# Optimization experiments

Hardware: AMD Instinct MI355X
Metric: run time of the kernel (lower is better)

Reference implementation:

```python
import jax, jax.numpy as jnp
import numpy as np

B, S, D = 2, 2048, 4096
H, G, HD = 32, 8, 128          # num_heads, num_kv_groups, head_dim
GROUP = H // G                  # group_size = 4
SCALE = HD ** -0.5


def setup_inputs() -> dict:
    key = jax.random.key(0)
    ks = jax.random.split(key, 6)
    x = jax.random.normal(ks[0], (B, S, D), dtype=jnp.float32)
    # Linear weights stored as [in, out] (y = x @ W), no bias, 0.02 init scale
    Wq = jax.random.normal(ks[1], (D, H * HD), dtype=jnp.float32) * 0.02
    Wk = jax.random.normal(ks[2], (D, G * HD), dtype=jnp.float32) * 0.02
    Wv = jax.random.normal(ks[3], (D, G * HD), dtype=jnp.float32) * 0.02
    Wo = jax.random.normal(ks[4], (H * HD, D), dtype=jnp.float32) * 0.02
    # RoPE tables: [S, HD], duplicated-half layout (rotate-half convention)
    inv_freq = 1.0 / (10000.0 ** (jnp.arange(0, HD, 2, dtype=jnp.float32) / HD))
    angles = jnp.arange(S, dtype=jnp.float32)[:, None] * inv_freq[None, :]  # [S, HD/2]
    angles = jnp.concatenate([angles, angles], axis=-1)                      # [S, HD]
    cos = jnp.cos(angles)
    sin = jnp.sin(angles)
    # causal mask: True = masked (strict upper triangle)
    mask = jnp.triu(jnp.ones((S, S), dtype=bool), k=1)
    return {"x": x, "Wq": Wq, "Wk": Wk, "Wv": Wv, "Wo": Wo,
            "cos": cos, "sin": sin, "mask": mask, "start_pos": 0}


def _rope(t, cos, sin, offset):
    # t: [B, h, S, HD]; cos/sin: [S_total, HD]
    n = t.shape[2]
    c = jax.lax.dynamic_slice_in_dim(cos, offset, n, axis=0)  # [n, HD]
    s = jax.lax.dynamic_slice_in_dim(sin, offset, n, axis=0)
    t1, t2 = t[..., : HD // 2], t[..., HD // 2:]
    rotated = jnp.concatenate([-t2, t1], axis=-1)
    return t * c[None, None] + rotated * s[None, None]


def reference(x, Wq, Wk, Wv, Wo, cos, sin, mask, start_pos):
    # projections
    q = (x @ Wq).reshape(B, S, H, HD).transpose(0, 2, 1, 3)   # [B,H,S,HD]
    k = (x @ Wk).reshape(B, S, G, HD).transpose(0, 2, 1, 3)   # [B,G,S,HD]
    v = (x @ Wv).reshape(B, S, G, HD).transpose(0, 2, 1, 3)   # [B,G,S,HD]
    # RoPE (no cache: prev_len = 0)
    q = _rope(q, cos, sin, start_pos) * SCALE
    k = _rope(k, cos, sin, start_pos)
    # GQA: expand kv groups to full heads (repeat_interleave along head dim)
    k_r = jnp.repeat(k, GROUP, axis=1)                         # [B,H,S,HD]
    v_r = jnp.repeat(v, GROUP, axis=1)
    scores = jnp.einsum('bhqd,bhkd->bhqk', q, k_r)             # [B,H,S,S]
    scores = jnp.where(mask[None, None], -jnp.inf, scores)
    w = jax.nn.softmax(scores, axis=-1)
    ctx = jnp.einsum('bhqk,bhkd->bhqd', w, v_r)                # [B,H,S,HD]
    ctx = ctx.transpose(0, 2, 1, 3).reshape(B, S, H * HD)
    out = ctx @ Wo                                             # [B,S,D]
    return out
```

## Files before the change

kernel.cpp:

```cpp
#include <hip/hip_runtime.h>
#include <hip/hip_bf16.h>
#include <math.h>

#define B_ 2
#define S_ 2048
#define D_ 4096
#define H_ 32
#define G_ 8
#define HD_ 128
#define GROUP_ 4
#define KVSTR_ (2 * G_ * HD_)
#define SCALE_ 0.08838834764831845f

typedef short bfv8 __attribute__((ext_vector_type(8)));
typedef float f32x4 __attribute__((ext_vector_type(4)));

__device__ __forceinline__ f32x4 mfma16(bfv8 a, bfv8 b, f32x4 c) {
  return __builtin_amdgcn_mfma_f32_16x16x32_bf16(a, b, c, 0, 0, 0);
}

__device__ __forceinline__ ushort f2bf_bits(float f) {
  __hip_bfloat16 h = __float2bfloat16(f);
  return *reinterpret_cast<ushort*>(&h);
}

__device__ __forceinline__ void gload16(const short* g, short* l) {
  __builtin_amdgcn_global_load_lds(
      (const __attribute__((address_space(1))) void*)g,
      (__attribute__((address_space(3))) void*)l, 16, 0, 0);
}

__global__ __launch_bounds__(256) void k_cvt(const float* __restrict__ in,
                                             ushort* __restrict__ out, int n4) {
  int i = blockIdx.x * 256 + threadIdx.x;
  if (i >= n4) return;
  float4 v = *(const float4*)(in + (size_t)i * 4);
  ushort4 o;
  o.x = f2bf_bits(v.x); o.y = f2bf_bits(v.y); o.z = f2bf_bits(v.z); o.w = f2bf_bits(v.w);
  *(ushort4*)(out + (size_t)i * 4) = o;
}

__global__ __launch_bounds__(256) void k_transpose(const float* __restrict__ in,
                                                   ushort* __restrict__ out,
                                                   int R, int C) {
  __shared__ ushort tile[32][36];
  int bc = blockIdx.x * 32;
  int br = blockIdx.y * 32;
  int t = threadIdx.x;
  int rr = t >> 3;
  int c4 = (t & 7) * 4;
  float4 v = *(const float4*)(in + (size_t)(br + rr) * C + bc + c4);
  tile[rr][c4 + 0] = f2bf_bits(v.x);
  tile[rr][c4 + 1] = f2bf_bits(v.y);
  tile[rr][c4 + 2] = f2bf_bits(v.z);
  tile[rr][c4 + 3] = f2bf_bits(v.w);
  __syncthreads();
  int cc = t >> 3;
  int r4 = (t & 7) * 4;
  ushort4 o;
  o.x = tile[r4 + 0][cc];
  o.y = tile[r4 + 1][cc];
  o.z = tile[r4 + 2][cc];
  o.w = tile[r4 + 3][cc];
  *(ushort4*)(out + (size_t)(bc + cc) * R + br + r4) = o;
}

__global__ __launch_bounds__(256) void k_transpose_v(const ushort* __restrict__ v,
                                                     ushort* __restrict__ vt,
                                                     int hstride, int hoff) {
  __shared__ ushort tile[32][33];
  int bg = blockIdx.z;
  int b = bg / G_, g = bg % G_;
  int s0 = blockIdx.y * 32;
  int h0 = blockIdx.x * 32;
  int tx = threadIdx.x, ty = threadIdx.y;
  const ushort* src = v + (size_t)b * S_ * hstride + (size_t)(hoff + g) * HD_;
  ushort* dst = vt + (size_t)(b * G_ + g) * HD_ * S_;
  for (int ii = 0; ii < 4; ii++) {
    int i = ty + ii * 8;
    tile[i][tx] = src[(size_t)(s0 + i) * hstride + h0 + tx];
  }
  __syncthreads();
  for (int ii = 0; ii < 4; ii++) {
    int i = ty + ii * 8;
    dst[(size_t)(h0 + i) * S_ + s0 + tx] = tile[tx][i];
  }
}

__global__ __launch_bounds__(256) void k_rope(__hip_bfloat16* __restrict__ t,
                                              const float* __restrict__ cosb,
                                              const float* __restrict__ sinb,
                                              int hstride, int nlaunch, float scale) {
  int item = blockIdx.x * 4 + (threadIdx.x >> 6);
  int head = item % nlaunch;
  int row = item / nlaunch;
  int s = row & (S_ - 1);
  int l = threadIdx.x & 63;
  size_t base = (size_t)row * hstride * HD_ + (size_t)head * HD_;
  float x1 = __bfloat162float(t[base + l]);
  float x2 = __bfloat162float(t[base + 64 + l]);
  float c1 = cosb[s * HD_ + l];
  float sn1 = sinb[s * HD_ + l];
  float c2 = cosb[s * HD_ + 64 + l];
  float sn2 = sinb[s * HD_ + 64 + l];
  t[base + l] = __float2bfloat16((x1 * c1 - x2 * sn1) * scale);
  t[base + 64 + l] = __float2bfloat16((x2 * c2 + x1 * sn2) * scale);
}

template <typename OT>
__global__ __launch_bounds__(256) void k_gemm_bt(const __hip_bfloat16* __restrict__ Ab,
                                                 const __hip_bfloat16* __restrict__ BTb,
                                                 OT* __restrict__ Cb,
                                                 int M, int N, int K) {
  __shared__ short sA[128 * 32];
  __shared__ short sB[128 * 32];
  int t = threadIdx.x;
  int w = t >> 6;
  int l = t & 63;
  int row0 = blockIdx.y * 128;
  int col0 = blockIdx.x * 128;
  int wr = (w >> 1) * 64;
  int wc = (w & 1) * 64;
  int fr = l & 15;
  int fq = l >> 4;
  int fo = fq * 8;
  int srow = l >> 2;
  int schk = (l & 3) * 8;

  const short* gA = (const short*)Ab;
  const short* gB = (const short*)BTb;

  f32x4 acc[4][4];
#pragma unroll
  for (int m = 0; m < 4; m++)
#pragma unroll
    for (int n = 0; n < 4; n++) acc[m][n] = (f32x4){0.f, 0.f, 0.f, 0.f};

  for (int k0 = 0; k0 < K; k0 += 32) {
    __syncthreads();
#pragma unroll
    for (int j = 0; j < 2; j++) {
      int r = w * 32 + j * 16;
      gload16(gA + (size_t)(row0 + r + srow) * K + k0 + schk, &sA[r * 32]);
      gload16(gB + (size_t)(col0 + r + srow) * K + k0 + schk, &sB[r * 32]);
    }
    __syncthreads();
    bfv8 af[4], bff[4];
#pragma unroll
    for (int m = 0; m < 4; m++) af[m] = *(const bfv8*)(sA + (wr + m * 16 + fr) * 32 + fo);
#pragma unroll
    for (int n = 0; n < 4; n++) bff[n] = *(const bfv8*)(sB + (wc + n * 16 + fr) * 32 + fo);
#pragma unroll
    for (int m = 0; m < 4; m++)
#pragma unroll
      for (int n = 0; n < 4; n++)
        acc[m][n] = mfma16(af[m], bff[n], acc[m][n]);
  }
#pragma unroll
  for (int m = 0; m < 4; m++)
#pragma unroll
    for (int n = 0; n < 4; n++)
#pragma unroll
      for (int j = 0; j < 4; j++) {
        int r = row0 + wr + m * 16 + fq * 4 + j;
        int c = col0 + wc + n * 16 + fr;
        if constexpr (__is_same(OT, float)) {
          Cb[(size_t)r * N + c] = acc[m][n][j];
        } else {
          Cb[(size_t)r * N + c] = __float2bfloat16(acc[m][n][j]);
        }
      }
}

template <typename OT>
__global__ __launch_bounds__(512, 2) void k_gemm256(const __hip_bfloat16* __restrict__ Ab,
                                                    const __hip_bfloat16* __restrict__ BTb,
                                                    OT* __restrict__ Cb,
                                                    int M, int N, int K) {
  __shared__ short sA[2][2][8192];
  __shared__ short sB[2][2][8192];
  int bid = blockIdx.x;
  int lg = (bid & 7) * 32 + (bid >> 3);
  int bx = lg >> 4;
  int by = lg & 15;
  int tid = threadIdx.x;
  int wid = tid >> 6;
  int l = tid & 63;
  int wr = (wid >> 2) * 128;
  int wc = (wid & 3) * 64;
  int fr = l & 15, fq = l >> 4;
  int cswz = (fq ^ ((fr >> 1) & 3)) * 8;
  int row0 = by * 256, col0 = bx * 256;
  int sr = l >> 2;
  int schunk = ((l & 3) ^ (((wid * 16 + sr) >> 1) & 3)) * 8;
  const short* gA = (const short*)Ab;
  const short* gB = (const short*)BTb;

  f32x4 acc[8][4];
#pragma unroll
  for (int m = 0; m < 8; m++)
#pragma unroll
    for (int n = 0; n < 4; n++) acc[m][n] = (f32x4){0.f, 0.f, 0.f, 0.f};

#define STAGE256(buf, kh, isB, kt)                                                   \
  {                                                                                  \
    const short* g_ = (isB) ? gB : gA;                                               \
    int b0_ = (isB) ? col0 : row0;                                                   \
    short* s_ = (isB) ? &sB[buf][kh][0] : &sA[buf][kh][0];                           \
    int k0_ = (kt) * 64 + (kh) * 32;                                                 \
    _Pragma("unroll")                                                                \
    for (int i_ = 0; i_ < 2; i_++) {                                                 \
      int r_ = i_ * 128 + wid * 16 + sr;                                             \
      gload16(g_ + (size_t)(b0_ + r_) * K + k0_ + schunk,                            \
              s_ + (i_ * 128 + wid * 16) * 32);                                      \
    }                                                                                \
  }

  bfv8 bf[4];
#define COMPUTE256(cur, kh, mg, loadB)                                               \
  {                                                                                  \
    if (loadB) {                                                                     \
      _Pragma("unroll")                                                              \
      for (int n_ = 0; n_ < 4; n_++)                                                 \
        bf[n_] = *(const bfv8*)&sB[cur][kh][(wc + n_ * 16 + fr) * 32 + cswz];        \
    }                                                                                \
    bfv8 af_[4];                                                                     \
    _Pragma("unroll")                                                                \
    for (int j_ = 0; j_ < 4; j_++)                                                   \
      af_[j_] = *(const bfv8*)&sA[cur][kh][(wr + ((mg) * 4 + j_) * 16 + fr) * 32 + cswz]; \
    __builtin_amdgcn_s_setprio(1);                                                   \
    _Pragma("unroll")                                                                \
    for (int j_ = 0; j_ < 4; j_++)                                                   \
      _Pragma("unroll")                                                              \
      for (int n_ = 0; n_ < 4; n_++)                                                 \
        acc[(mg) * 4 + j_][n_] = mfma16(af_[j_], bf[n_], acc[(mg) * 4 + j_][n_]);    \
    __builtin_amdgcn_s_setprio(0);                                                   \
  }

  int NT = K / 64;
  STAGE256(0, 0, false, 0);
  STAGE256(0, 0, true, 0);
  STAGE256(0, 1, false, 0);
  STAGE256(0, 1, true, 0);

  for (int t = 0; t < NT - 1; t++) {
    int cur = t & 1, nxt = cur ^ 1;
    asm volatile("s_waitcnt vmcnt(4)" ::: "memory");
    __builtin_amdgcn_s_barrier();
    STAGE256(nxt, 0, false, t + 1);
    COMPUTE256(cur, 0, 0, true);
    STAGE256(nxt, 0, true, t + 1);
    COMPUTE256(cur, 0, 1, false);
    asm volatile("s_waitcnt vmcnt(4)" ::: "memory");
    __builtin_amdgcn_s_barrier();
    STAGE256(nxt, 1, false, t + 1);
    COMPUTE256(cur, 1, 0, true);
    STAGE256(nxt, 1, true, t + 1);
    COMPUTE256(cur, 1, 1, false);
  }
  {
    int cur = (NT - 1) & 1;
    asm volatile("s_waitcnt vmcnt(4)" ::: "memory");
    __builtin_amdgcn_s_barrier();
    COMPUTE256(cur, 0, 0, true);
    COMPUTE256(cur, 0, 1, false);
    asm volatile("s_waitcnt vmcnt(0)" ::: "memory");
    __builtin_amdgcn_s_barrier();
    COMPUTE256(cur, 1, 0, true);
    COMPUTE256(cur, 1, 1, false);
  }
#undef STAGE256
#undef COMPUTE256

#pragma unroll
  for (int m = 0; m < 8; m++)
#pragma unroll
    for (int n = 0; n < 4; n++)
#pragma unroll
      for (int j = 0; j < 4; j++) {
        int r = row0 + wr + m * 16 + fq * 4 + j;
        int c = col0 + wc + n * 16 + fr;
        if constexpr (__is_same(OT, float)) {
          Cb[(size_t)r * N + c] = acc[m][n][j];
        } else {
          Cb[(size_t)r * N + c] = __float2bfloat16(acc[m][n][j]);
        }
      }
}

#define PSTR 68
__global__ __launch_bounds__(512) void k_attn5(const __hip_bfloat16* __restrict__ Qb,
                                               const __hip_bfloat16* __restrict__ KVb,
                                               const __hip_bfloat16* __restrict__ VTb,
                                               __hip_bfloat16* __restrict__ ctx) {
  __shared__ short sK[64 * 128];
  __shared__ short sV[128 * 64];
  __shared__ short sP[8][16 * PSTR];

  const int nQB = S_ / 128;
  int blk = blockIdx.x;
  int qb = (nQB - 1) - (blk % nQB);
  int bh = blk / nQB;
  int h = bh % H_;
  int b = bh / H_;
  int g = h / GROUP_;
  int q0 = qb * 128;

  int t = threadIdx.x;
  int wid = t >> 6;
  int l = t & 63;
  int fr = l & 15, fq = l >> 4, fo = fq * 8;
  int wq0 = q0 + wid * 16;

  const short* qp = (const short*)Qb + (size_t)b * S_ * H_ * HD_ + (size_t)h * HD_;
  const short* kp = (const short*)KVb + (size_t)b * S_ * KVSTR_ + (size_t)g * HD_;
  const short* vp = (const short*)VTb + (size_t)(b * G_ + g) * HD_ * S_;

  bfv8 qf[4];
#pragma unroll
  for (int c = 0; c < 4; c++)
    qf[c] = *(const bfv8*)(qp + (size_t)(wq0 + fr) * (H_ * HD_) + c * 32 + fo);

  f32x4 acc[8];
#pragma unroll
  for (int n = 0; n < 8; n++) acc[n] = (f32x4){0.f, 0.f, 0.f, 0.f};
  float m[4], ll[4];
#pragma unroll
  for (int j = 0; j < 4; j++) { m[j] = -INFINITY; ll[j] = 0.f; }

  int krow_i = l >> 4;
  int kchk = l & 15;
  int vrow_i = l >> 3;
  int vchk = l & 7;

#define STAGE_K(k0s)                                                                 \
  _Pragma("unroll")                                                                  \
  for (int j = 0; j < 2; j++) {                                                      \
    int base = wid * 8 + j * 4;                                                      \
    int r = base + krow_i;                                                           \
    gload16(kp + (size_t)((k0s) + r) * KVSTR_ + ((kchk ^ (r & 7)) * 8),              \
            &sK[base * 128]);                                                        \
  }
#define STAGE_V(k0s)                                                                 \
  _Pragma("unroll")                                                                  \
  for (int j = 0; j < 2; j++) {                                                      \
    int base = wid * 16 + j * 8;                                                     \
    int r = base + vrow_i;                                                           \
    gload16(vp + (size_t)r * S_ + (k0s) + ((vchk ^ (r & 7)) * 8), &sV[base * 64]);   \
  }

  int nkt = 2 * qb + 2;
  STAGE_K(0);
  STAGE_V(0);

  for (int kt = 0; kt < nkt; kt++) {
    int k0 = kt * 64;
    bool wactive = (k0 <= wq0 + 15);
    bool needmask = (k0 + 63 > wq0);

    asm volatile("s_waitcnt vmcnt(2)" ::: "memory");
    __builtin_amdgcn_s_barrier();

    float p[4][4];
    if (wactive) {
      f32x4 sf[4];
#pragma unroll
      for (int ks = 0; ks < 4; ks++) {
        sf[ks] = (f32x4){0.f, 0.f, 0.f, 0.f};
        int row = ks * 16 + fr;
        int rx = row & 7;
#pragma unroll
        for (int c = 0; c < 4; c++) {
          bfv8 kf = *(const bfv8*)&sK[row * 128 + (((c * 4 + fq) ^ rx) * 8)];
          sf[ks] = mfma16(qf[c], kf, sf[ks]);
        }
      }

      float sc[4], red[4];
      if (needmask) {
#pragma unroll
        for (int j = 0; j < 4; j++) {
          int q = wq0 + fq * 4 + j;
#pragma unroll
          for (int ks = 0; ks < 4; ks++)
            if (k0 + ks * 16 + fr > q) sf[ks][j] = -INFINITY;
        }
      }
#pragma unroll
      for (int j = 0; j < 4; j++)
        red[j] = fmaxf(fmaxf(sf[0][j], sf[1][j]), fmaxf(sf[2][j], sf[3][j]));
#pragma unroll
      for (int off = 1; off < 16; off <<= 1)
#pragma unroll
        for (int j = 0; j < 4; j++)
          red[j] = fmaxf(red[j], __shfl_xor(red[j], off, 64));
#pragma unroll
      for (int j = 0; j < 4; j++) {
        float nm = fmaxf(m[j], red[j]);
        sc[j] = __expf(m[j] - nm);
        m[j] = nm;
#pragma unroll
        for (int ks = 0; ks < 4; ks++) p[ks][j] = __expf(sf[ks][j] - nm);
        red[j] = (p[0][j] + p[1][j]) + (p[2][j] + p[3][j]);
      }
#pragma unroll
      for (int off = 1; off < 16; off <<= 1)
#pragma unroll
        for (int j = 0; j < 4; j++)
          red[j] += __shfl_xor(red[j], off, 64);
#pragma unroll
      for (int j = 0; j < 4; j++) {
        ll[j] = ll[j] * sc[j] + red[j];
#pragma unroll
        for (int n = 0; n < 8; n++) acc[n][j] *= sc[j];
#pragma unroll
        for (int ks = 0; ks < 4; ks++)
          sP[wid][(fq * 4 + j) * PSTR + ks * 16 + fr] = f2bf_bits(p[ks][j]);
      }
    }

    asm volatile("s_waitcnt vmcnt(0)" ::: "memory");
    __builtin_amdgcn_s_barrier();
    if (kt + 1 < nkt) STAGE_K(k0 + 64);

    if (wactive) {
      bfv8 pa0 = *(const bfv8*)&sP[wid][fr * PSTR + fo];
      bfv8 pa1 = *(const bfv8*)&sP[wid][fr * PSTR + 32 + fo];
#pragma unroll
      for (int n = 0; n < 8; n++) {
        int row = n * 16 + fr;
        int rx = row & 7;
        bfv8 vf0 = *(const bfv8*)&sV[row * 64 + ((fq ^ rx) * 8)];
        bfv8 vf1 = *(const bfv8*)&sV[row * 64 + (((4 + fq) ^ rx) * 8)];
        acc[n] = mfma16(pa0, vf0, acc[n]);
        acc[n] = mfma16(pa1, vf1, acc[n]);
      }
    }

    if (kt + 1 < nkt) {
      __builtin_amdgcn_s_barrier();
      STAGE_V(k0 + 64);
    }
  }
#undef STAGE_K
#undef STAGE_V

#pragma unroll
  for (int n = 0; n < 8; n++)
#pragma unroll
    for (int j = 0; j < 4; j++) {
      int q = wq0 + fq * 4 + j;
      float o = acc[n][j] / ll[j];
      ctx[(size_t)(b * S_ + q) * (H_ * HD_) + h * HD_ + n * 16 + fr] = __float2bfloat16(o);
    }
}

extern "C" void kernel_launch(void* const* d_in, const int* in_sizes, int n_in,
                              void* d_out, int out_size, void* d_ws, size_t ws_size,
                              hipStream_t stream) {
  (void)in_sizes; (void)n_in; (void)out_size; (void)ws_size;
  const float* x    = (const float*)d_in[0];
  const float* Wq   = (const float*)d_in[1];
  const float* Wk   = (const float*)d_in[2];
  const float* Wv   = (const float*)d_in[3];
  const float* Wo   = (const float*)d_in[4];
  const float* cosb = (const float*)d_in[5];
  const float* sinb = (const float*)d_in[6];

  char* ws = (char*)d_ws;
  __hip_bfloat16* xb  = (__hip_bfloat16*)(ws + 0);
  __hip_bfloat16* WqT = (__hip_bfloat16*)(ws + 33554432);
  __hip_bfloat16* WkT = (__hip_bfloat16*)(ws + 67108864);
  __hip_bfloat16* WvT = (__hip_bfloat16*)(ws + 75497472);
  __hip_bfloat16* Qb  = (__hip_bfloat16*)(ws + 83886080);
  __hip_bfloat16* KVb = (__hip_bfloat16*)(ws + 117440512);
  __hip_bfloat16* VTb = (__hip_bfloat16*)(ws + 134217728);
  __hip_bfloat16* Cx  = xb;

  k_cvt<<<(B_ * S_ * D_ / 4 + 255) / 256, 256, 0, stream>>>(x, (ushort*)xb, B_ * S_ * D_ / 4);
  k_transpose<<<dim3(128, 128), 256, 0, stream>>>(Wq, (ushort*)WqT, 4096, 4096);
  k_transpose<<<dim3(32, 128), 256, 0, stream>>>(Wk, (ushort*)WkT, 4096, 1024);
  k_transpose<<<dim3(32, 128), 256, 0, stream>>>(Wv, (ushort*)WvT, 4096, 1024);

  k_gemm256<__hip_bfloat16><<<256, 512, 0, stream>>>(xb, WqT, Qb, 4096, 4096, 4096);
  k_gemm_bt<__hip_bfloat16><<<dim3(16, 32), 256, 0, stream>>>(xb, WkT, KVb, 4096, 2048, 4096);

  k_transpose<<<dim3(128, 128), 256, 0, stream>>>(Wo, (ushort*)WqT, 4096, 4096);

  k_rope<<<4096 * 32 / 4, 256, 0, stream>>>(Qb, cosb, sinb, 32, 32, SCALE_);
  k_rope<<<4096 * 8 / 4, 256, 0, stream>>>((__hip_bfloat16*)KVb, cosb, sinb, 16, 8, 1.0f);

  k_transpose_v<<<dim3(4, 64, 16), dim3(32, 8), 0, stream>>>((const ushort*)KVb, (ushort*)VTb,
                                                             KVSTR_, G_);

  k_attn5<<<B_ * H_ * (S_ / 128), 512, 0, stream>>>(Qb, KVb, VTb, Cx);

  k_gemm256<float><<<256, 512, 0, stream>>>(Cx, WqT, (float*)d_out, 4096, 4096, 4096);
}
```

Before: 724.1 us.

## Split GEMM inner loop into barrier-separated LDS-load and MFMA phases

Restructures the 256-tile GEMM main loop into explicit phases: LDS fragment loads plus global staging, then a barrier and lgkmcnt wait, then an MFMA cluster, then another barrier. The aim is to keep waves in lockstep so memory and matrix phases of different waves interleave (ping-pong style) and LDS latency is hidden. It adds many extra workgroup barriers per k-step, which may stall waves if the phases are unbalanced. The global-to-LDS wait placement also changes, and the correctness of reading the next buffer relies on the new barrier ordering.

```diff
diff --git a/kernel.cpp b/kernel.cpp
--- a/kernel.cpp
+++ b/kernel.cpp
@@ -216,18 +216,21 @@
     }                                                                                \
   }
 
-  bfv8 bf[4];
-#define COMPUTE256(cur, kh, mg, loadB)                                               \
+  bfv8 bf[4], af_[4];
+#define PH_DSLOAD(cur, kh, mg, loadB)                                                \
   {                                                                                  \
     if (loadB) {                                                                     \
       _Pragma("unroll")                                                              \
       for (int n_ = 0; n_ < 4; n_++)                                                 \
         bf[n_] = *(const bfv8*)&sB[cur][kh][(wc + n_ * 16 + fr) * 32 + cswz];        \
     }                                                                                \
-    bfv8 af_[4];                                                                     \
     _Pragma("unroll")                                                                \
     for (int j_ = 0; j_ < 4; j_++)                                                   \
       af_[j_] = *(const bfv8*)&sA[cur][kh][(wr + ((mg) * 4 + j_) * 16 + fr) * 32 + cswz]; \
+  }
+
+#define PH_MFMA(mg)                                                                  \
+  {                                                                                  \
     __builtin_amdgcn_s_setprio(1);                                                   \
     _Pragma("unroll")                                                                \
     for (int j_ = 0; j_ < 4; j_++)                                                   \
@@ -242,35 +245,61 @@
   STAGE256(0, 0, true, 0);
   STAGE256(0, 1, false, 0);
   STAGE256(0, 1, true, 0);
+  asm volatile("s_waitcnt vmcnt(4)" ::: "memory");
+  __builtin_amdgcn_s_barrier();
 
   for (int t = 0; t < NT - 1; t++) {
     int cur = t & 1, nxt = cur ^ 1;
+    PH_DSLOAD(cur, 0, 0, true);
+    STAGE256(nxt, 0, false, t + 1);
+    __builtin_amdgcn_s_barrier();
+    asm volatile("s_waitcnt lgkmcnt(0)" ::: "memory");
+    PH_MFMA(0);
+    __builtin_amdgcn_s_barrier();
+    PH_DSLOAD(cur, 0, 1, false);
+    STAGE256(nxt, 0, true, t + 1);
     asm volatile("s_waitcnt vmcnt(4)" ::: "memory");
     __builtin_amdgcn_s_barrier();
-    STAGE256(nxt, 0, false, t + 1);
-    COMPUTE256(cur, 0, 0, true);
-    STAGE256(nxt, 0, true, t + 1);
-    COMPUTE256(cur, 0, 1, false);
+    asm volatile("s_waitcnt lgkmcnt(0)" ::: "memory");
+    PH_MFMA(1);
+    __builtin_amdgcn_s_barrier();
+    PH_DSLOAD(cur, 1, 0, true);
+    STAGE256(nxt, 1, false, t + 1);
+    __builtin_amdgcn_s_barrier();
+    asm volatile("s_waitcnt lgkmcnt(0)" ::: "memory");
+    PH_MFMA(0);
+    __builtin_amdgcn_s_barrier();
+    PH_DSLOAD(cur, 1, 1, false);
+    STAGE256(nxt, 1, true, t + 1);
     asm volatile("s_waitcnt vmcnt(4)" ::: "memory");
     __builtin_amdgcn_s_barrier();
-    STAGE256(nxt, 1, false, t + 1);
-    COMPUTE256(cur, 1, 0, true);
-    STAGE256(nxt, 1, true, t + 1);
-    COMPUTE256(cur, 1, 1, false);
+    asm volatile("s_waitcnt lgkmcnt(0)" ::: "memory");
+    PH_MFMA(1);
+    __builtin_amdgcn_s_barrier();
   }
   {
     int cur = (NT - 1) & 1;
-    asm volatile("s_waitcnt vmcnt(4)" ::: "memory");
-    __builtin_amdgcn_s_barrier();
-    COMPUTE256(cur, 0, 0, true);
-    COMPUTE256(cur, 0, 1, false);
+    PH_DSLOAD(cur, 0, 0, true);
+    __builtin_amdgcn_s_barrier();
+    asm volatile("s_waitcnt lgkmcnt(0)" ::: "memory");
+    PH_MFMA(0);
+    __builtin_amdgcn_s_barrier();
+    PH_DSLOAD(cur, 0, 1, false);
     asm volatile("s_waitcnt vmcnt(0)" ::: "memory");
     __builtin_amdgcn_s_barrier();
-    COMPUTE256(cur, 1, 0, true);
-    COMPUTE256(cur, 1, 1, false);
+    asm volatile("s_waitcnt lgkmcnt(0)" ::: "memory");
+    PH_MFMA(1);
+    __builtin_amdgcn_s_barrier();
+    PH_DSLOAD(cur, 1, 0, true);
+    asm volatile("s_waitcnt lgkmcnt(0)" ::: "memory");
+    PH_MFMA(0);
+    PH_DSLOAD(cur, 1, 1, false);
+    asm volatile("s_waitcnt lgkmcnt(0)" ::: "memory");
+    PH_MFMA(1);
   }
 #undef STAGE256
-#undef COMPUTE256
+#undef PH_DSLOAD
+#undef PH_MFMA
 
 #pragma unroll
   for (int m = 0; m < 8; m++)
```

Result: no change. 738.3 us (+2.0%).
